# Kernel tuning notes

Measured on AMD Instinct MI355X. Metric: run time of the kernel, lower is better.

The kernel has to match this reference:

```python
import jax, jax.numpy as jnp
import numpy as np

B, W, M, HD, RL, RD = 32, 32, 1024, 64, 2, 32
D = RL * HD  # concat of per-layer hidden states


def setup_inputs() -> dict:
    key = jax.random.key(0)
    ks = jax.random.split(key, 16)
    s = 0.1
    r = lambda k, shape: (jax.random.normal(k, shape, jnp.float32) * s)
    return {
        "x_input": jax.random.normal(ks[0], (B, W, M), jnp.float32),
        "major_graph": jax.random.normal(ks[1], (M, M), jnp.float32) * 0.02,
        "H_init": jnp.zeros((RL, M, HD), jnp.float32),
        # GRU layer 0: input size 1 -> hidden HD
        "Wih0": r(ks[2], (3 * HD, 1)),
        "Whh0": r(ks[3], (3 * HD, HD)),
        "bih0": jnp.zeros((3 * HD,), jnp.float32),
        "bhh0": jnp.zeros((3 * HD,), jnp.float32),
        # GRU layer 1: hidden HD -> hidden HD
        "Wih1": r(ks[4], (3 * HD, HD)),
        "Whh1": r(ks[5], (3 * HD, HD)),
        "bih1": jnp.zeros((3 * HD,), jnp.float32),
        "bhh1": jnp.zeros((3 * HD,), jnp.float32),
        # weight-normed Linear(RL*HD -> RD)
        "V": r(ks[6], (RD, D)),
        "g": jnp.ones((RD,), jnp.float32),
        "b_lin": jnp.zeros((RD,), jnp.float32),
        # FinalRowWise layer: per-node weights [M, RD] -> scalar per node
        "W_fr": r(ks[7], (M, RD)),
        "b_fr": jnp.zeros((M,), jnp.float32),
    }


def _gru_cell(x, h, Wih, Whh, bih, bhh):
    # x: [B, M, in], h: [B, M, HD]
    gi = x @ Wih.T + bih
    gh = h @ Whh.T + bhh
    ir, iz, inn = jnp.split(gi, 3, axis=-1)
    hr, hz, hnn = jnp.split(gh, 3, axis=-1)
    rgate = jax.nn.sigmoid(ir + hr)
    zgate = jax.nn.sigmoid(iz + hz)
    n = jnp.tanh(inn + rgate * hnn)
    return (1.0 - zgate) * n + zgate * h


def reference(x_input, major_graph, H_init, Wih0, Whh0, bih0, bhh0,
              Wih1, Whh1, bih1, bhh1, V, g, b_lin, W_fr, b_fr):
    Bn, Wn_, Mn = x_input.shape
    # h0: [RL, B, M, HD] (H_init broadcast over batch)
    h0 = jnp.broadcast_to(H_init[:, None], (H_init.shape[0], Bn, Mn, H_init.shape[-1]))
    # weight_norm (dim=0): per-output-row normalization of V scaled by g
    Wn = g[:, None] * V / jnp.linalg.norm(V, axis=1, keepdims=True)  # [RD, D]
    x_seq = jnp.transpose(x_input, (1, 0, 2))[..., None]  # [W, B, M, 1]

    def step(hn, x_t):
        hn0 = _gru_cell(x_t, hn, Wih0, Whh0, bih0, bhh0)        # [B, M, HD]
        hn1 = _gru_cell(hn0, h0[1], Wih1, Whh1, bih1, bhh1)     # [B, M, HD] (fresh h0 each step, as in source)
        x_p = jnp.concatenate([hn0, hn1], axis=-1)              # [B, M, D]
        # graph-weighted projection along node axis: x_p @ major_graph
        x_g = jax.nn.relu(jnp.einsum('bid,ij->bjd', x_p, major_graph))  # [B, M, D]
        y = jax.nn.sigmoid(x_g @ Wn.T + b_lin)                  # [B, M, RD]
        out = jnp.einsum('bmd,md->bm', y, W_fr) + b_fr          # [B, M]
        return hn1, out

    _, outs = jax.lax.scan(step, h0[0], x_seq)  # [W, B, M]
    return jnp.transpose(outs, (1, 0, 2))       # [B, W, M]
```

## Files before the change

kernel.cpp:

```cpp
#include <hip/hip_runtime.h>
#include <math.h>

#define B_  32
#define W_  32
#define M_  1024
#define HD_ 64
#define RD_ 32
#define D_  128
#define CH_ 16
#define NKT 32

typedef short bf16x8 __attribute__((ext_vector_type(8)));
typedef float f32x4  __attribute__((ext_vector_type(4)));

#define AS1 __attribute__((address_space(1)))
#define AS3 __attribute__((address_space(3)))

__device__ __forceinline__ void gload16(const void* g, void* l) {
    __builtin_amdgcn_global_load_lds((const AS1 void*)g, (AS3 void*)l, 16, 0, 0);
}

__device__ __forceinline__ unsigned short f2b(float f) {
    unsigned int u = __float_as_uint(f);
    u += 0x7fffu + ((u >> 16) & 1u);
    return (unsigned short)(u >> 16);
}
__device__ __forceinline__ float b2f(unsigned short h) {
    return __uint_as_float(((unsigned int)h) << 16);
}
__device__ __forceinline__ float sigf(float x) { return 1.0f / (1.0f + __expf(-x)); }
__device__ __forceinline__ float tanhf_(float x) { return 2.0f / (1.0f + __expf(-2.0f * x)) - 1.0f; }


__global__ __launch_bounds__(256) void gt_kernel(const float* __restrict__ G,
                                                 unsigned short* __restrict__ GTb) {
    __shared__ float T[64][65];
    int i0 = blockIdx.x * 64, j0 = blockIdx.y * 64;
    int tid = threadIdx.x;
    int r = tid >> 4, c4 = (tid & 15) * 4;
    #pragma unroll
    for (int q = 0; q < 4; ++q) {
        float4 v = *(const float4*)&G[(i0 + r + q * 16) * M_ + j0 + c4];
        T[r + q * 16][c4] = v.x; T[r + q * 16][c4 + 1] = v.y;
        T[r + q * 16][c4 + 2] = v.z; T[r + q * 16][c4 + 3] = v.w;
    }
    __syncthreads();
    #pragma unroll
    for (int q = 0; q < 4; ++q) {
        int jr = r + q * 16;
        ushort4 o;
        o.x = f2b(T[c4][jr]); o.y = f2b(T[c4 + 1][jr]);
        o.z = f2b(T[c4 + 2][jr]); o.w = f2b(T[c4 + 3][jr]);
        *(ushort4*)&GTb[(j0 + jr) * M_ + i0 + c4] = o;
    }
}

__global__ __launch_bounds__(192) void gh1ct_kernel(const float* __restrict__ H_init,
                                                    const float* __restrict__ Whh1,
                                                    const float* __restrict__ bhh1,
                                                    float* __restrict__ gh1cT) {
    int m = blockIdx.x, k = threadIdx.x;
    __shared__ float h01[HD_];
    if (k < HD_) h01[k] = H_init[(M_ + m) * HD_ + k];
    __syncthreads();
    float d = 0.f;
    #pragma unroll
    for (int hd = 0; hd < HD_; ++hd) d = fmaf(h01[hd], Whh1[k * HD_ + hd], d);
    gh1cT[k * M_ + m] = d + bhh1[k];
}

__global__ __launch_bounds__(128) void wn_kernel(const float* __restrict__ V,
                                                 const float* __restrict__ g,
                                                 unsigned short* __restrict__ Wnb) {
    int r = blockIdx.x, d = threadIdx.x;
    float v = V[r * D_ + d];
    float s = v * v;
    #pragma unroll
    for (int off = 32; off > 0; off >>= 1) s += __shfl_down(s, off);
    __shared__ float ws[2];
    if ((threadIdx.x & 63) == 0) ws[threadIdx.x >> 6] = s;
    __syncthreads();
    float norm = sqrtf(ws[0] + ws[1]);
    Wnb[r * D_ + d] = f2b(g[r] * v / norm);
}

__global__ __launch_bounds__(256) void castw_kernel(const float* __restrict__ Whh0,
                                                    const float* __restrict__ Wih1,
                                                    unsigned short* __restrict__ Whh0b,
                                                    unsigned short* __restrict__ Wih1b) {
    int i = blockIdx.x * 256 + threadIdx.x;
    Whh0b[i] = f2b(Whh0[i]);
    Wih1b[i] = f2b(Wih1[i]);
}

__global__ __launch_bounds__(256) void inith_kernel(const float* __restrict__ H_init,
                                                    unsigned short* __restrict__ Hb) {
    int e8 = blockIdx.x * 256 + threadIdx.x;
    int base = e8 * 8;
    int src = base & (M_ * HD_ - 1);
    float4 v0 = *(const float4*)&H_init[src];
    float4 v1 = *(const float4*)&H_init[src + 4];
    uint4 u;
    u.x = (unsigned int)f2b(v0.x) | ((unsigned int)f2b(v0.y) << 16);
    u.y = (unsigned int)f2b(v0.z) | ((unsigned int)f2b(v0.w) << 16);
    u.z = (unsigned int)f2b(v1.x) | ((unsigned int)f2b(v1.y) << 16);
    u.w = (unsigned int)f2b(v1.z) | ((unsigned int)f2b(v1.w) << 16);
    *(uint4*)&Hb[base] = u;
}

__global__ __launch_bounds__(256) void gru_chunk_kernel(
    const float* __restrict__ x_input, const float* __restrict__ Wih0,
    const float* __restrict__ bih0, const float* __restrict__ bhh0,
    const unsigned short* __restrict__ Whh0b, const unsigned short* __restrict__ Wih1b,
    const float* __restrict__ bih1, const float* __restrict__ gh1cT,
    const float* __restrict__ H_init, unsigned short* __restrict__ Hb,
    unsigned short* __restrict__ XPT_c, int t0)
{
    __shared__ unsigned short Whh0s[192 * 64];
    __shared__ unsigned short Wih1s[192 * 64];
    __shared__ unsigned short hn0s[64 * 64];
    __shared__ unsigned short hn1s[64 * 64];
    const int tid = threadIdx.x, w = tid >> 6, l = tid & 63;
    const int li = l & 15, lh = l >> 4;
    const int b = blockIdx.x >> 4, mt = blockIdx.x & 15;
    const int m0 = mt * 64;
    const int p0b = b * M_ + m0;
    const int ms = m0 + w * 16;

    for (int i = tid; i < 1536; i += 256) {
        int row = i >> 3, pos = i & 7, sc = pos ^ (row & 7);
        gload16(&Whh0b[row * 64 + sc * 8], (char*)Whh0s + (i & ~63) * 16);
        gload16(&Wih1b[row * 64 + sc * 8], (char*)Wih1s + (i & ~63) * 16);
    }
    for (int idx = tid; idx < 512; idx += 256) {
        int p = idx >> 3, cc = idx & 7;
        uint4 v = *(const uint4*)&Hb[(p0b + p) * HD_ + cc * 8];
        *(uint4*)((char*)hn1s + p * 128 + ((cc ^ (p & 7)) << 4)) = v;
    }

    float wi_[3][4], bi0_[3][4], bh0_[3][4], bi1_[3][4];
    float vrA[4][4], vzA[4][4], vnA[4][4], h01A[4][4];
    #pragma unroll
    for (int fi = 0; fi < 4; ++fi) {
        int ko = li + 16 * fi;
        #pragma unroll
        for (int g3 = 0; g3 < 3; ++g3) {
            wi_[g3][fi]  = Wih0[g3 * 64 + ko];
            bi0_[g3][fi] = bih0[g3 * 64 + ko];
            bh0_[g3][fi] = bhh0[g3 * 64 + ko];
            bi1_[g3][fi] = bih1[g3 * 64 + ko];
        }
        float4 vr = *(const float4*)&gh1cT[(ko) * M_ + ms + lh * 4];
        float4 vz = *(const float4*)&gh1cT[(64 + ko) * M_ + ms + lh * 4];
        float4 vn = *(const float4*)&gh1cT[(128 + ko) * M_ + ms + lh * 4];
        vrA[fi][0] = vr.x; vrA[fi][1] = vr.y; vrA[fi][2] = vr.z; vrA[fi][3] = vr.w;
        vzA[fi][0] = vz.x; vzA[fi][1] = vz.y; vzA[fi][2] = vz.z; vzA[fi][3] = vz.w;
        vnA[fi][0] = vn.x; vnA[fi][1] = vn.y; vnA[fi][2] = vn.z; vnA[fi][3] = vn.w;
        #pragma unroll
        for (int reg = 0; reg < 4; ++reg)
            h01A[fi][reg] = H_init[M_ * HD_ + (ms + lh * 4 + reg) * HD_ + ko];
    }

    __syncthreads();
    float hst[4][4];
    #pragma unroll
    for (int fi = 0; fi < 4; ++fi) {
        int ko = li + 16 * fi;
        #pragma unroll
        for (int reg = 0; reg < 4; ++reg) {
            int ml = w * 16 + lh * 4 + reg;
            hst[fi][reg] = b2f(*(const unsigned short*)((char*)hn1s + ml * 128 +
                               ((((ko >> 3) ^ (ml & 7))) << 4) + (ko & 7) * 2));
        }
    }

    for (int ts = 0; ts < CH_; ++ts) {
        int t = t0 + ts;
        __syncthreads();

        float4 xv = *(const float4*)&x_input[(b * W_ + t) * M_ + ms + lh * 4];
        float x4[4] = {xv.x, xv.y, xv.z, xv.w};

        bf16x8 a0_0, a0_1;
        {
            int row = w * 16 + li;
            a0_0 = *(const bf16x8*)((char*)hn1s + row * 128 + ((lh ^ (row & 7)) << 4));
            a0_1 = *(const bf16x8*)((char*)hn1s + row * 128 + (((4 + lh) ^ (row & 7)) << 4));
        }
        f32x4 acc[12];
        #pragma unroll
        for (int nt = 0; nt < 12; ++nt) acc[nt] = (f32x4){0.f, 0.f, 0.f, 0.f};
        #pragma unroll
        for (int nt = 0; nt < 12; ++nt) {
            int row = nt * 16 + li;
            bf16x8 b0 = *(const bf16x8*)((char*)Whh0s + row * 128 + ((lh ^ (row & 7)) << 4));
            bf16x8 b1 = *(const bf16x8*)((char*)Whh0s + row * 128 + (((4 + lh) ^ (row & 7)) << 4));
            acc[nt] = __builtin_amdgcn_mfma_f32_16x16x32_bf16(a0_0, b0, acc[nt], 0, 0, 0);
            acc[nt] = __builtin_amdgcn_mfma_f32_16x16x32_bf16(a0_1, b1, acc[nt], 0, 0, 0);
        }
        #pragma unroll
        for (int reg = 0; reg < 4; ++reg) {
            int ml = w * 16 + lh * 4 + reg;
            #pragma unroll
            for (int fi = 0; fi < 4; ++fi) {
                int j = li + 16 * fi;
                float hprev = hst[fi][reg];
                float gr = acc[fi][reg]     + bh0_[0][fi];
                float gz = acc[4 + fi][reg] + bh0_[1][fi];
                float gn = acc[8 + fi][reg] + bh0_[2][fi];
                float x = x4[reg];
                float r = sigf(x * wi_[0][fi] + bi0_[0][fi] + gr);
                float z = sigf(x * wi_[1][fi] + bi0_[1][fi] + gz);
                float n = tanhf_(x * wi_[2][fi] + bi0_[2][fi] + r * gn);
                float h0v = (1.f - z) * n + z * hprev;
                *(unsigned short*)((char*)hn0s + ml * 128 +
                    ((((j >> 3) ^ (ml & 7))) << 4) + (j & 7) * 2) = f2b(h0v);
            }
        }
        __syncthreads();

        bf16x8 a1_0, a1_1;
        {
            int row = w * 16 + li;
            a1_0 = *(const bf16x8*)((char*)hn0s + row * 128 + ((lh ^ (row & 7)) << 4));
            a1_1 = *(const bf16x8*)((char*)hn0s + row * 128 + (((4 + lh) ^ (row & 7)) << 4));
        }
        #pragma unroll
        for (int nt = 0; nt < 12; ++nt) acc[nt] = (f32x4){0.f, 0.f, 0.f, 0.f};
        #pragma unroll
        for (int nt = 0; nt < 12; ++nt) {
            int row = nt * 16 + li;
            bf16x8 b0 = *(const bf16x8*)((char*)Wih1s + row * 128 + ((lh ^ (row & 7)) << 4));
            bf16x8 b1 = *(const bf16x8*)((char*)Wih1s + row * 128 + (((4 + lh) ^ (row & 7)) << 4));
            acc[nt] = __builtin_amdgcn_mfma_f32_16x16x32_bf16(a1_0, b0, acc[nt], 0, 0, 0);
            acc[nt] = __builtin_amdgcn_mfma_f32_16x16x32_bf16(a1_1, b1, acc[nt], 0, 0, 0);
        }
        #pragma unroll
        for (int fi = 0; fi < 4; ++fi) {
            int ko = li + 16 * fi;
            #pragma unroll
            for (int reg = 0; reg < 4; ++reg) {
                int ml = w * 16 + lh * 4 + reg;
                float r = sigf(acc[fi][reg]     + bi1_[0][fi] + vrA[fi][reg]);
                float z = sigf(acc[4 + fi][reg] + bi1_[1][fi] + vzA[fi][reg]);
                float n = tanhf_(acc[8 + fi][reg] + bi1_[2][fi] + r * vnA[fi][reg]);
                float h1v = (1.f - z) * n + z * h01A[fi][reg];
                hst[fi][reg] = h1v;
                *(unsigned short*)((char*)hn1s + ml * 128 +
                    ((((ko >> 3) ^ (ml & 7))) << 4) + (ko & 7) * 2) = f2b(h1v);
            }
        }
        __syncthreads();

        {
            unsigned short* XPT = XPT_c + (size_t)ts * (D_ * B_ * M_);
            int d = tid >> 1, mh = (tid & 1) * 32;
            const char* src = (d < 64) ? (const char*)hn0s : (const char*)hn1s;
            int dd = d & 63;
            unsigned int pk[16];
            #pragma unroll
            for (int mm = 0; mm < 32; mm += 2) {
                int ma = mh + mm, mb = mh + mm + 1;
                unsigned int ua = *(const unsigned short*)(src + ma * 128 + (((dd >> 3) ^ (ma & 7)) << 4) + (dd & 7) * 2);
                unsigned int ub = *(const unsigned short*)(src + mb * 128 + (((dd >> 3) ^ (mb & 7)) << 4) + (dd & 7) * 2);
                pk[mm >> 1] = ua | (ub << 16);
            }
            #pragma unroll
            for (int q = 0; q < 4; ++q) {
                uint4 o = {pk[q * 4], pk[q * 4 + 1], pk[q * 4 + 2], pk[q * 4 + 3]};
                *(uint4*)&XPT[(b * D_ + d) * M_ + m0 + mh + q * 8] = o;
            }
        }
    }

    #pragma unroll
    for (int it = 0; it < 2; ++it) {
        int idx = tid + it * 256;
        int p = idx >> 3, cc = idx & 7;
        uint4 v = *(const uint4*)((char*)hn1s + p * 128 + ((cc ^ (p & 7)) << 4));
        *(uint4*)&Hb[(p0b + p) * HD_ + cc * 8] = v;
    }
}

__global__ __launch_bounds__(512, 2) void gemmhead_kernel(
    const unsigned short* __restrict__ GTb, const unsigned short* __restrict__ XPT_c,
    const unsigned short* __restrict__ Wnb, const float* __restrict__ b_lin,
    const float* __restrict__ W_fr, const float* __restrict__ b_fr,
    float* __restrict__ out, int t0)
{
    __shared__ __align__(16) char lds[131072];
    const int tid = threadIdx.x, w = tid >> 6, l = tid & 63;
    const int li = l & 15, lh = l >> 4;
    const int wm = w >> 2, wn = w & 3;
    const int ntile = blockIdx.x >> 2;
    const int j0 = (blockIdx.x & 3) * 256;
    const unsigned short* Asrc = GTb + (size_t)j0 * M_;
    const unsigned short* Bsrc = XPT_c + (size_t)ntile * 256 * M_;

    f32x4 acc[8][4];
    #pragma unroll
    for (int mi = 0; mi < 8; ++mi)
        #pragma unroll
        for (int ni = 0; ni < 4; ++ni) acc[mi][ni] = (f32x4){0.f, 0.f, 0.f, 0.f};

    #define STAGE_A(kt, c) { \
        _Pragma("unroll") \
        for (int rr = 0; rr < 2; ++rr) { \
            int i = rr * 512 + tid; \
            int row = i >> 2, pos = i & 3, sc = pos ^ (row & 3); \
            gload16(&Asrc[row * M_ + (kt) * 32 + sc * 8], lds + (c) * 32768 + (i & ~63) * 16); \
        } }
    #define STAGE_B(kt, c) { \
        _Pragma("unroll") \
        for (int rr = 0; rr < 2; ++rr) { \
            int i = rr * 512 + tid; \
            int row = i >> 2, pos = i & 3, sc = pos ^ (row & 3); \
            gload16(&Bsrc[row * M_ + (kt) * 32 + sc * 8], lds + (c) * 32768 + 16384 + (i & ~63) * 16); \
        } }

    STAGE_A(0, 0); STAGE_B(0, 0);
    STAGE_A(1, 1); STAGE_B(1, 1);

    for (int kt = 0; kt < NKT; ++kt) {
        if (kt < NKT - 1) { asm volatile("s_waitcnt vmcnt(4)" ::: "memory"); }
        else              { asm volatile("s_waitcnt vmcnt(0)" ::: "memory"); }
        __builtin_amdgcn_s_barrier();
        asm volatile("" ::: "memory");
        const int cur = kt % 3;
        const char* Abuf = lds + cur * 32768;
        const char* Bbuf = lds + cur * 32768 + 16384;
        bf16x8 afr[8], bfr[4];
        #pragma unroll
        for (int ni = 0; ni < 4; ++ni) {
            int row = wn * 64 + ni * 16 + li;
            bfr[ni] = *(const bf16x8*)(Bbuf + row * 64 + ((lh ^ (row & 3)) << 4));
        }
        #pragma unroll
        for (int mi = 0; mi < 4; ++mi) {
            int row = wm * 128 + mi * 16 + li;
            afr[mi] = *(const bf16x8*)(Abuf + row * 64 + ((lh ^ (row & 3)) << 4));
        }
        if (kt + 2 < NKT) STAGE_A(kt + 2, (kt + 2) % 3);
        __builtin_amdgcn_s_setprio(1);
        #pragma unroll
        for (int mi = 0; mi < 4; ++mi)
            #pragma unroll
            for (int ni = 0; ni < 4; ++ni)
                acc[mi][ni] = __builtin_amdgcn_mfma_f32_16x16x32_bf16(afr[mi], bfr[ni], acc[mi][ni], 0, 0, 0);
        __builtin_amdgcn_s_setprio(0);
        __builtin_amdgcn_s_barrier();
        asm volatile("" ::: "memory");
        #pragma unroll
        for (int mi = 4; mi < 8; ++mi) {
            int row = wm * 128 + mi * 16 + li;
            afr[mi] = *(const bf16x8*)(Abuf + row * 64 + ((lh ^ (row & 3)) << 4));
        }
        if (kt + 2 < NKT) STAGE_B(kt + 2, (kt + 2) % 3);
        __builtin_amdgcn_s_setprio(1);
        #pragma unroll
        for (int mi = 4; mi < 8; ++mi)
            #pragma unroll
            for (int ni = 0; ni < 4; ++ni)
                acc[mi][ni] = __builtin_amdgcn_mfma_f32_16x16x32_bf16(afr[mi], bfr[ni], acc[mi][ni], 0, 0, 0);
        __builtin_amdgcn_s_setprio(0);
    }

    __syncthreads();

    #pragma unroll
    for (int mi = 0; mi < 8; ++mi)
        #pragma unroll
        for (int ni = 0; ni < 4; ++ni)
            #pragma unroll
            for (int reg = 0; reg < 4; ++reg) {
                int jl = wm * 128 + mi * 16 + lh * 4 + reg;
                int cl = wn * 64 + ni * 16 + li;
                float v = fmaxf(acc[mi][ni][reg], 0.f);
                int byte = jl * 512 + ((((cl >> 3) ^ (jl & 7))) << 4) + (cl & 7) * 2;
                *(unsigned short*)(lds + byte) = f2b(v);
            }
    __syncthreads();

    const int ts = ntile >> 4, b0 = (ntile & 15) * 2;
    const int t = t0 + ts;
    float bl0 = b_lin[li], bl1 = b_lin[16 + li];
    #pragma unroll
    for (int rg = 0; rg < 2; ++rg) {
        int row = w * 32 + rg * 16 + li;
        #pragma unroll
        for (int p = 0; p < 2; ++p) {
            f32x4 P0 = (f32x4){0.f, 0.f, 0.f, 0.f};
            f32x4 P1 = (f32x4){0.f, 0.f, 0.f, 0.f};
            #pragma unroll
            for (int ks = 0; ks < 4; ++ks) {
                int cp = (p * 16 + ks * 4 + lh) ^ (row & 7);
                bf16x8 xa = *(const bf16x8*)(lds + row * 512 + cp * 16);
                bf16x8 wb0 = *(const bf16x8*)&Wnb[(li) * D_ + ks * 32 + lh * 8];
                bf16x8 wb1 = *(const bf16x8*)&Wnb[(16 + li) * D_ + ks * 32 + lh * 8];
                P0 = __builtin_amdgcn_mfma_f32_16x16x32_bf16(xa, wb0, P0, 0, 0, 0);
                P1 = __builtin_amdgcn_mfma_f32_16x16x32_bf16(xa, wb1, P1, 0, 0, 0);
            }
            float s[4];
            #pragma unroll
            for (int reg = 0; reg < 4; ++reg) {
                int j = j0 + w * 32 + rg * 16 + lh * 4 + reg;
                float y0 = sigf(P0[reg] + bl0);
                float y1 = sigf(P1[reg] + bl1);
                s[reg] = y0 * W_fr[j * RD_ + li] + y1 * W_fr[j * RD_ + 16 + li];
            }
            #pragma unroll
            for (int off = 1; off < 16; off <<= 1) {
                #pragma unroll
                for (int reg = 0; reg < 4; ++reg) s[reg] += __shfl_xor(s[reg], off);
            }
            if (li == 0) {
                int jb = j0 + w * 32 + rg * 16 + lh * 4;
                float4 o = {s[0] + b_fr[jb], s[1] + b_fr[jb + 1],
                            s[2] + b_fr[jb + 2], s[3] + b_fr[jb + 3]};
                *(float4*)&out[((b0 + p) * W_ + t) * M_ + jb] = o;
            }
        }
    }
}


extern "C" void kernel_launch(void* const* d_in, const int* in_sizes, int n_in,
                              void* d_out, int out_size, void* d_ws, size_t ws_size,
                              hipStream_t stream) {
    const float* x_input = (const float*)d_in[0];
    const float* G       = (const float*)d_in[1];
    const float* H_init  = (const float*)d_in[2];
    const float* Wih0    = (const float*)d_in[3];
    const float* Whh0    = (const float*)d_in[4];
    const float* bih0    = (const float*)d_in[5];
    const float* bhh0    = (const float*)d_in[6];
    const float* Wih1    = (const float*)d_in[7];
    const float* Whh1    = (const float*)d_in[8];
    const float* bih1    = (const float*)d_in[9];
    const float* bhh1    = (const float*)d_in[10];
    const float* V       = (const float*)d_in[11];
    const float* gvec    = (const float*)d_in[12];
    const float* b_lin   = (const float*)d_in[13];
    const float* W_fr    = (const float*)d_in[14];
    const float* b_fr    = (const float*)d_in[15];
    float* out = (float*)d_out;

    char* ws = (char*)d_ws;
    unsigned short* GTb   = (unsigned short*)(ws);
    unsigned short* XPT_c = (unsigned short*)(ws + (2u   << 20));
    unsigned short* Hb    = (unsigned short*)(ws + (130u << 20));
    float*          gh1cT = (float*)(ws + (134u << 20));
    unsigned short* Wnb   = (unsigned short*)(ws + (135u << 20));
    unsigned short* Whh0b = (unsigned short*)(ws + (135u << 20) + 8192);
    unsigned short* Wih1b = (unsigned short*)(ws + (135u << 20) + 8192 + 24576);

    gt_kernel   <<<dim3(16, 16), 256, 0, stream>>>(G, GTb);
    gh1ct_kernel<<<M_, 192, 0, stream>>>(H_init, Whh1, bhh1, gh1cT);
    wn_kernel   <<<RD_, 128, 0, stream>>>(V, gvec, Wnb);
    castw_kernel<<<48, 256, 0, stream>>>(Whh0, Wih1, Whh0b, Wih1b);
    inith_kernel<<<1024, 256, 0, stream>>>(H_init, Hb);

    for (int c = 0; c < W_ / CH_; ++c) {
        gru_chunk_kernel<<<512, 256, 0, stream>>>(x_input, Wih0, bih0, bhh0, Whh0b,
                                                  Wih1b, bih1, gh1cT, H_init, Hb,
                                                  XPT_c, c * CH_);
        gemmhead_kernel<<<dim3(1024), 512, 0, stream>>>(GTb, XPT_c, Wnb, b_lin,
                                                        W_fr, b_fr, out, c * CH_);
    }
}
```

Measured before the change: 630.4 us.

## Shrink graph GEMM tiles, double-buffer BK64, and make GRU rows wave-private to drop barriers

The graph GEMM+head kernel goes from 256x256 output tiles with BK=32 triple buffering to 128x128 tiles with BK=64 double buffering. It launches 4x more blocks with 64KB LDS and a higher occupancy bound, and the block index is remapped so blocks sharing a B tile run close together. In the GRU chunk kernel, each wave now owns its own 16 rows for loading, storing and transposing hidden state, so all per-step __syncthreads are removed. Smaller tiles give more parallelism and occupancy but reload A and B from global memory more often, with more per-block overhead.

```diff
diff --git a/kernel.cpp b/kernel.cpp
--- a/kernel.cpp
+++ b/kernel.cpp
@@ -8,7 +8,7 @@
 #define RD_ 32
 #define D_  128
 #define CH_ 16
-#define NKT 32
+#define NKT 16
 
 typedef short bf16x8 __attribute__((ext_vector_type(8)));
 typedef float f32x4  __attribute__((ext_vector_type(4)));
@@ -132,10 +132,14 @@
         gload16(&Whh0b[row * 64 + sc * 8], (char*)Whh0s + (i & ~63) * 16);
         gload16(&Wih1b[row * 64 + sc * 8], (char*)Wih1s + (i & ~63) * 16);
     }
-    for (int idx = tid; idx < 512; idx += 256) {
-        int p = idx >> 3, cc = idx & 7;
-        uint4 v = *(const uint4*)&Hb[(p0b + p) * HD_ + cc * 8];
-        *(uint4*)((char*)hn1s + p * 128 + ((cc ^ (p & 7)) << 4)) = v;
+    {
+        int p = w * 16 + (l >> 2);
+        #pragma unroll
+        for (int q = 0; q < 2; ++q) {
+            int cc = (l & 3) * 2 + q;
+            uint4 v = *(const uint4*)&Hb[(p0b + p) * HD_ + cc * 8];
+            *(uint4*)((char*)hn1s + p * 128 + ((cc ^ (p & 7)) << 4)) = v;
+        }
     }
 
     float wi_[3][4], bi0_[3][4], bh0_[3][4], bi1_[3][4];
@@ -162,6 +166,7 @@
     }
 
     __syncthreads();
+
     float hst[4][4];
     #pragma unroll
     for (int fi = 0; fi < 4; ++fi) {
@@ -176,8 +181,6 @@
 
     for (int ts = 0; ts < CH_; ++ts) {
         int t = t0 + ts;
-        __syncthreads();
-
         float4 xv = *(const float4*)&x_input[(b * W_ + t) * M_ + ms + lh * 4];
         float x4[4] = {xv.x, xv.y, xv.z, xv.w};
 
@@ -217,7 +220,6 @@
                     ((((j >> 3) ^ (ml & 7))) << 4) + (j & 7) * 2) = f2b(h0v);
             }
         }
-        __syncthreads();
 
         bf16x8 a1_0, a1_1;
         {
@@ -250,175 +252,165 @@
                     ((((ko >> 3) ^ (ml & 7))) << 4) + (ko & 7) * 2) = f2b(h1v);
             }
         }
-        __syncthreads();
 
         {
             unsigned short* XPT = XPT_c + (size_t)ts * (D_ * B_ * M_);
-            int d = tid >> 1, mh = (tid & 1) * 32;
-            const char* src = (d < 64) ? (const char*)hn0s : (const char*)hn1s;
-            int dd = d & 63;
-            unsigned int pk[16];
-            #pragma unroll
-            for (int mm = 0; mm < 32; mm += 2) {
-                int ma = mh + mm, mb = mh + mm + 1;
-                unsigned int ua = *(const unsigned short*)(src + ma * 128 + (((dd >> 3) ^ (ma & 7)) << 4) + (dd & 7) * 2);
-                unsigned int ub = *(const unsigned short*)(src + mb * 128 + (((dd >> 3) ^ (mb & 7)) << 4) + (dd & 7) * 2);
-                pk[mm >> 1] = ua | (ub << 16);
+            unsigned int pk[8];
+            #pragma unroll
+            for (int r2 = 0; r2 < 16; r2 += 2) {
+                int ma = w * 16 + r2, mb = ma + 1;
+                unsigned int ua = *(const unsigned short*)((char*)hn0s + ma * 128 + (((l >> 3) ^ (ma & 7)) << 4) + (l & 7) * 2);
+                unsigned int ub = *(const unsigned short*)((char*)hn0s + mb * 128 + (((l >> 3) ^ (mb & 7)) << 4) + (l & 7) * 2);
+                pk[r2 >> 1] = ua | (ub << 16);
             }
-            #pragma unroll
-            for (int q = 0; q < 4; ++q) {
-                uint4 o = {pk[q * 4], pk[q * 4 + 1], pk[q * 4 + 2], pk[q * 4 + 3]};
-                *(uint4*)&XPT[(b * D_ + d) * M_ + m0 + mh + q * 8] = o;
+            uint4 o0 = {pk[0], pk[1], pk[2], pk[3]};
+            uint4 o1 = {pk[4], pk[5], pk[6], pk[7]};
+            *(uint4*)&XPT[(b * D_ + l) * M_ + ms]     = o0;
+            *(uint4*)&XPT[(b * D_ + l) * M_ + ms + 8] = o1;
+            #pragma unroll
+            for (int r2 = 0; r2 < 16; r2 += 2) {
+                int ma = w * 16 + r2, mb = ma + 1;
+                unsigned int ua = *(const unsigned short*)((char*)hn1s + ma * 128 + (((l >> 3) ^ (ma & 7)) << 4) + (l & 7) * 2);
+                unsigned int ub = *(const unsigned short*)((char*)hn1s + mb * 128 + (((l >> 3) ^ (mb & 7)) << 4) + (l & 7) * 2);
+                pk[r2 >> 1] = ua | (ub << 16);
             }
-        }
-    }
-
-    #pragma unroll
-    for (int it = 0; it < 2; ++it) {
-        int idx = tid + it * 256;
-        int p = idx >> 3, cc = idx & 7;
-        uint4 v = *(const uint4*)((char*)hn1s + p * 128 + ((cc ^ (p & 7)) << 4));
-        *(uint4*)&Hb[(p0b + p) * HD_ + cc * 8] = v;
-    }
-}
-
-__global__ __launch_bounds__(512, 2) void gemmhead_kernel(
+            uint4 o2 = {pk[0], pk[1], pk[2], pk[3]};
+            uint4 o3 = {pk[4], pk[5], pk[6], pk[7]};
+            *(uint4*)&XPT[(b * D_ + 64 + l) * M_ + ms]     = o2;
+            *(uint4*)&XPT[(b * D_ + 64 + l) * M_ + ms + 8] = o3;
+        }
+    }
+
+    {
+        int p = w * 16 + (l >> 2);
+        #pragma unroll
+        for (int q = 0; q < 2; ++q) {
+            int cc = (l & 3) * 2 + q;
+            uint4 v = *(const uint4*)((char*)hn1s + p * 128 + ((cc ^ (p & 7)) << 4));
+            *(uint4*)&Hb[(p0b + p) * HD_ + cc * 8] = v;
+        }
+    }
+}
+
+__global__ __launch_bounds__(512, 4) void gemmhead_kernel(
     const unsigned short* __restrict__ GTb, const unsigned short* __restrict__ XPT_c,
     const unsigned short* __restrict__ Wnb, const float* __restrict__ b_lin,
     const float* __restrict__ W_fr, const float* __restrict__ b_fr,
     float* __restrict__ out, int t0)
 {
-    __shared__ __align__(16) char lds[131072];
+    __shared__ __align__(16) char lds[65536];
     const int tid = threadIdx.x, w = tid >> 6, l = tid & 63;
     const int li = l & 15, lh = l >> 4;
     const int wm = w >> 2, wn = w & 3;
-    const int ntile = blockIdx.x >> 2;
-    const int j0 = (blockIdx.x & 3) * 256;
+    const int bid = blockIdx.x;
+    const int ntile = (bid & 7) + ((bid >> 6) << 3);
+    const int j0 = ((bid >> 3) & 7) * 128;
     const unsigned short* Asrc = GTb + (size_t)j0 * M_;
-    const unsigned short* Bsrc = XPT_c + (size_t)ntile * 256 * M_;
-
-    f32x4 acc[8][4];
-    #pragma unroll
-    for (int mi = 0; mi < 8; ++mi)
-        #pragma unroll
-        for (int ni = 0; ni < 4; ++ni) acc[mi][ni] = (f32x4){0.f, 0.f, 0.f, 0.f};
-
-    #define STAGE_A(kt, c) { \
+    const unsigned short* Bsrc = XPT_c + (size_t)ntile * 128 * M_;
+
+    f32x4 acc[4][2];
+    #pragma unroll
+    for (int mi = 0; mi < 4; ++mi)
+        #pragma unroll
+        for (int ni = 0; ni < 2; ++ni) acc[mi][ni] = (f32x4){0.f, 0.f, 0.f, 0.f};
+
+    #define STAGE(kt, c) { \
         _Pragma("unroll") \
-        for (int rr = 0; rr < 2; ++rr) { \
-            int i = rr * 512 + tid; \
-            int row = i >> 2, pos = i & 3, sc = pos ^ (row & 3); \
-            gload16(&Asrc[row * M_ + (kt) * 32 + sc * 8], lds + (c) * 32768 + (i & ~63) * 16); \
+        for (int q = 0; q < 2; ++q) { \
+            int i = q * 512 + tid; \
+            int row = i >> 3, pos = i & 7, sc = pos ^ (row & 7); \
+            gload16(&Asrc[row * M_ + (kt) * 64 + sc * 8], lds + (c) * 32768 + (i & ~63) * 16); \
+            gload16(&Bsrc[row * M_ + (kt) * 64 + sc * 8], lds + (c) * 32768 + 16384 + (i & ~63) * 16); \
         } }
-    #define STAGE_B(kt, c) { \
-        _Pragma("unroll") \
-        for (int rr = 0; rr < 2; ++rr) { \
-            int i = rr * 512 + tid; \
-            int row = i >> 2, pos = i & 3, sc = pos ^ (row & 3); \
-            gload16(&Bsrc[row * M_ + (kt) * 32 + sc * 8], lds + (c) * 32768 + 16384 + (i & ~63) * 16); \
-        } }
-
-    STAGE_A(0, 0); STAGE_B(0, 0);
-    STAGE_A(1, 1); STAGE_B(1, 1);
+
+    STAGE(0, 0);
 
     for (int kt = 0; kt < NKT; ++kt) {
-        if (kt < NKT - 1) { asm volatile("s_waitcnt vmcnt(4)" ::: "memory"); }
+        if (kt + 1 < NKT) { STAGE(kt + 1, (kt + 1) & 1);
+                            asm volatile("s_waitcnt vmcnt(4)" ::: "memory"); }
         else              { asm volatile("s_waitcnt vmcnt(0)" ::: "memory"); }
         __builtin_amdgcn_s_barrier();
         asm volatile("" ::: "memory");
-        const int cur = kt % 3;
-        const char* Abuf = lds + cur * 32768;
-        const char* Bbuf = lds + cur * 32768 + 16384;
-        bf16x8 afr[8], bfr[4];
-        #pragma unroll
-        for (int ni = 0; ni < 4; ++ni) {
-            int row = wn * 64 + ni * 16 + li;
-            bfr[ni] = *(const bf16x8*)(Bbuf + row * 64 + ((lh ^ (row & 3)) << 4));
-        }
+        const char* Abuf = lds + (kt & 1) * 32768;
+        const char* Bbuf = Abuf + 16384;
+        bf16x8 af[4][2], bfv[2][2];
         #pragma unroll
         for (int mi = 0; mi < 4; ++mi) {
-            int row = wm * 128 + mi * 16 + li;
-            afr[mi] = *(const bf16x8*)(Abuf + row * 64 + ((lh ^ (row & 3)) << 4));
-        }
-        if (kt + 2 < NKT) STAGE_A(kt + 2, (kt + 2) % 3);
+            int row = wm * 64 + mi * 16 + li;
+            #pragma unroll
+            for (int kk = 0; kk < 2; ++kk)
+                af[mi][kk] = *(const bf16x8*)(Abuf + row * 128 + (((kk * 4 + lh) ^ (row & 7)) << 4));
+        }
+        #pragma unroll
+        for (int ni = 0; ni < 2; ++ni) {
+            int row = wn * 32 + ni * 16 + li;
+            #pragma unroll
+            for (int kk = 0; kk < 2; ++kk)
+                bfv[ni][kk] = *(const bf16x8*)(Bbuf + row * 128 + (((kk * 4 + lh) ^ (row & 7)) << 4));
+        }
         __builtin_amdgcn_s_setprio(1);
         #pragma unroll
-        for (int mi = 0; mi < 4; ++mi)
-            #pragma unroll
-            for (int ni = 0; ni < 4; ++ni)
-                acc[mi][ni] = __builtin_amdgcn_mfma_f32_16x16x32_bf16(afr[mi], bfr[ni], acc[mi][ni], 0, 0, 0);
+        for (int kk = 0; kk < 2; ++kk)
+            #pragma unroll
+            for (int mi = 0; mi < 4; ++mi)
+                #pragma unroll
+                for (int ni = 0; ni < 2; ++ni)
+                    acc[mi][ni] = __builtin_amdgcn_mfma_f32_16x16x32_bf16(af[mi][kk], bfv[ni][kk], acc[mi][ni], 0, 0, 0);
         __builtin_amdgcn_s_setprio(0);
+        asm volatile("s_waitcnt lgkmcnt(0)" ::: "memory");
         __builtin_amdgcn_s_barrier();
         asm volatile("" ::: "memory");
-        #pragma unroll
-        for (int mi = 4; mi < 8; ++mi) {
-            int row = wm * 128 + mi * 16 + li;
-            afr[mi] = *(const bf16x8*)(Abuf + row * 64 + ((lh ^ (row & 3)) << 4));
-        }
-        if (kt + 2 < NKT) STAGE_B(kt + 2, (kt + 2) % 3);
-        __builtin_amdgcn_s_setprio(1);
-        #pragma unroll
-        for (int mi = 4; mi < 8; ++mi)
-            #pragma unroll
-            for (int ni = 0; ni < 4; ++ni)
-                acc[mi][ni] = __builtin_amdgcn_mfma_f32_16x16x32_bf16(afr[mi], bfr[ni], acc[mi][ni], 0, 0, 0);
-        __builtin_amdgcn_s_setprio(0);
-    }
-
-    __syncthreads();
-
-    #pragma unroll
-    for (int mi = 0; mi < 8; ++mi)
-        #pragma unroll
-        for (int ni = 0; ni < 4; ++ni)
+    }
+
+    __syncthreads();
+
+    #pragma unroll
+    for (int mi = 0; mi < 4; ++mi)
+        #pragma unroll
+        for (int ni = 0; ni < 2; ++ni)
             #pragma unroll
             for (int reg = 0; reg < 4; ++reg) {
-                int jl = wm * 128 + mi * 16 + lh * 4 + reg;
-                int cl = wn * 64 + ni * 16 + li;
+                int jl = wm * 64 + mi * 16 + lh * 4 + reg;
+                int cl = wn * 32 + ni * 16 + li;
                 float v = fmaxf(acc[mi][ni][reg], 0.f);
-                int byte = jl * 512 + ((((cl >> 3) ^ (jl & 7))) << 4) + (cl & 7) * 2;
+                int byte = jl * 256 + ((((cl >> 3) ^ (jl & 7))) << 4) + (cl & 7) * 2;
                 *(unsigned short*)(lds + byte) = f2b(v);
             }
     __syncthreads();
 
-    const int ts = ntile >> 4, b0 = (ntile & 15) * 2;
-    const int t = t0 + ts;
+    const int b = ntile & 31, t = t0 + (ntile >> 5);
     float bl0 = b_lin[li], bl1 = b_lin[16 + li];
-    #pragma unroll
-    for (int rg = 0; rg < 2; ++rg) {
-        int row = w * 32 + rg * 16 + li;
-        #pragma unroll
-        for (int p = 0; p < 2; ++p) {
-            f32x4 P0 = (f32x4){0.f, 0.f, 0.f, 0.f};
-            f32x4 P1 = (f32x4){0.f, 0.f, 0.f, 0.f};
-            #pragma unroll
-            for (int ks = 0; ks < 4; ++ks) {
-                int cp = (p * 16 + ks * 4 + lh) ^ (row & 7);
-                bf16x8 xa = *(const bf16x8*)(lds + row * 512 + cp * 16);
-                bf16x8 wb0 = *(const bf16x8*)&Wnb[(li) * D_ + ks * 32 + lh * 8];
-                bf16x8 wb1 = *(const bf16x8*)&Wnb[(16 + li) * D_ + ks * 32 + lh * 8];
-                P0 = __builtin_amdgcn_mfma_f32_16x16x32_bf16(xa, wb0, P0, 0, 0, 0);
-                P1 = __builtin_amdgcn_mfma_f32_16x16x32_bf16(xa, wb1, P1, 0, 0, 0);
-            }
-            float s[4];
-            #pragma unroll
-            for (int reg = 0; reg < 4; ++reg) {
-                int j = j0 + w * 32 + rg * 16 + lh * 4 + reg;
-                float y0 = sigf(P0[reg] + bl0);
-                float y1 = sigf(P1[reg] + bl1);
-                s[reg] = y0 * W_fr[j * RD_ + li] + y1 * W_fr[j * RD_ + 16 + li];
-            }
-            #pragma unroll
-            for (int off = 1; off < 16; off <<= 1) {
-                #pragma unroll
-                for (int reg = 0; reg < 4; ++reg) s[reg] += __shfl_xor(s[reg], off);
-            }
-            if (li == 0) {
-                int jb = j0 + w * 32 + rg * 16 + lh * 4;
-                float4 o = {s[0] + b_fr[jb], s[1] + b_fr[jb + 1],
-                            s[2] + b_fr[jb + 2], s[3] + b_fr[jb + 3]};
-                *(float4*)&out[((b0 + p) * W_ + t) * M_ + jb] = o;
-            }
+    {
+        int row = w * 16 + li;
+        f32x4 P0 = (f32x4){0.f, 0.f, 0.f, 0.f};
+        f32x4 P1 = (f32x4){0.f, 0.f, 0.f, 0.f};
+        #pragma unroll
+        for (int ks = 0; ks < 4; ++ks) {
+            int cp = (ks * 4 + lh) ^ (row & 7);
+            bf16x8 xa = *(const bf16x8*)(lds + row * 256 + cp * 16);
+            bf16x8 wb0 = *(const bf16x8*)&Wnb[(li) * D_ + ks * 32 + lh * 8];
+            bf16x8 wb1 = *(const bf16x8*)&Wnb[(16 + li) * D_ + ks * 32 + lh * 8];
+            P0 = __builtin_amdgcn_mfma_f32_16x16x32_bf16(xa, wb0, P0, 0, 0, 0);
+            P1 = __builtin_amdgcn_mfma_f32_16x16x32_bf16(xa, wb1, P1, 0, 0, 0);
+        }
+        float s[4];
+        #pragma unroll
+        for (int reg = 0; reg < 4; ++reg) {
+            int j = j0 + w * 16 + lh * 4 + reg;
+            float y0 = sigf(P0[reg] + bl0);
+            float y1 = sigf(P1[reg] + bl1);
+            s[reg] = y0 * W_fr[j * RD_ + li] + y1 * W_fr[j * RD_ + 16 + li];
+        }
+        #pragma unroll
+        for (int off = 1; off < 16; off <<= 1) {
+            #pragma unroll
+            for (int reg = 0; reg < 4; ++reg) s[reg] += __shfl_xor(s[reg], off);
+        }
+        if (li == 0) {
+            int jb = j0 + w * 16 + lh * 4;
+            float4 o = {s[0] + b_fr[jb], s[1] + b_fr[jb + 1],
+                        s[2] + b_fr[jb + 2], s[3] + b_fr[jb + 3]};
+            *(float4*)&out[(b * W_ + t) * M_ + jb] = o;
         }
     }
 }
@@ -464,7 +456,7 @@
         gru_chunk_kernel<<<512, 256, 0, stream>>>(x_input, Wih0, bih0, bhh0, Whh0b,
                                                   Wih1b, bih1, gh1cT, H_init, Hb,
                                                   XPT_c, c * CH_);
-        gemmhead_kernel<<<dim3(1024), 512, 0, stream>>>(GTb, XPT_c, Wnb, b_lin,
+        gemmhead_kernel<<<dim3(4096), 512, 0, stream>>>(GTb, XPT_c, Wnb, b_lin,
                                                         W_fr, b_fr, out, c * CH_);
     }
 }
```

Result: slower. 666.1 us (+5.7%).
